# Kernel optimization log

Measured on AMD Instinct MI355X. Metric: run time of the kernel, lower is better.

## Reference

```python
import jax, jax.numpy as jnp
import numpy as np

M = 20          # mixture components
T = 1.0         # temperature
LATENT = 128
STROKE = 5
IN_DIM = LATENT + STROKE   # conditional=False -> 133
H = 1024        # dec_hidden_dim
HY = 256        # dec_hyper_dim
F = 64          # feature_dim (hypernet embedding)
NSEQ = 128      # Nmax
B = 64          # batch_size
OUT_DIM = 6 * M + 3
SQRT_T = float(np.sqrt(T))


def _w(key, shape, fan):
    return jax.random.normal(key, shape, jnp.float32) * np.float32(1.0 / np.sqrt(fan))


def setup_inputs() -> dict:
    key = jax.random.key(0)
    ks = jax.random.split(key, 16)
    inp = {
        'z': jax.random.normal(ks[0], (B, LATENT), jnp.float32),
        'strokes': jax.random.normal(ks[1], (NSEQ, B, IN_DIM), jnp.float32),
        'fc_in_w': _w(ks[2], (LATENT, 2 * H + 2 * HY), LATENT),
        'fc_in_b': jnp.zeros((2 * H + 2 * HY,), jnp.float32),
        'fc_proj_w': _w(ks[3], (H, OUT_DIM), H),
        'fc_proj_b': jnp.zeros((OUT_DIM,), jnp.float32),
        'Wx': _w(ks[4], (IN_DIM, 4 * H), IN_DIM),
        'Wh': _w(ks[5], (H, 4 * H), H),
        'b0': jnp.zeros((4, H), jnp.float32),
        'Wxh_hy': _w(ks[6], (IN_DIM + H, 4 * HY), IN_DIM + H),
        'Whh_hy': _w(ks[7], (HY, 4 * HY), HY),
        'b_hy': jnp.zeros((4 * HY,), jnp.float32),
        'Wzx': _w(ks[8], (HY, 4 * F), HY),
        'bzx': jnp.ones((4 * F,), jnp.float32),
        'Wzh': _w(ks[9], (HY, 4 * F), HY),
        'bzh': jnp.ones((4 * F,), jnp.float32),
        'Wzb': _w(ks[10], (HY, 4 * F), HY),
        'Dx': _w(ks[11], (4, F, H), F),
        'Dh': _w(ks[12], (4, F, H), F),
        'Db': _w(ks[13], (4, F, H), F),
    }
    return inp


def _hyperlstm_mdn(z, strokes, fc_in_w, fc_in_b, fc_proj_w, fc_proj_b, Wx, Wh, b0,
                   Wxh_hy, Whh_hy, b_hy, Wzx, bzx, Wzh, bzh, Wzb, Dx, Dh, Db):
    # initial states: tanh(fc_in(z)) split into [H, H, HY, HY]
    s0 = jnp.tanh(z @ fc_in_w + fc_in_b)
    h0, c0, hh0, ch0 = jnp.split(s0, [H, 2 * H, 2 * H + HY], axis=1)

    def step(carry, x_t):
        h, c, hh, ch = carry
        # hyper LSTM: plain LSTM over concat(x, h_main)
        hx = jnp.concatenate([x_t, h], axis=1)          # (B, IN_DIM+H)
        g = hx @ Wxh_hy + hh @ Whh_hy + b_hy            # (B, 4*HY)
        hi, hf, hg, ho = jnp.split(g, 4, axis=1)
        ch = jax.nn.sigmoid(hf) * ch + jax.nn.sigmoid(hi) * jnp.tanh(hg)
        hh = jax.nn.sigmoid(ho) * jnp.tanh(ch)
        # hyper embeddings -> per-gate row scales of main LSTM weights
        zx = (hh @ Wzx + bzx).reshape(-1, 4, F)
        zh = (hh @ Wzh + bzh).reshape(-1, 4, F)
        zb = (hh @ Wzb).reshape(-1, 4, F)
        sx = jnp.einsum('bgf,gfh->bgh', zx, Dx)         # (B,4,H)
        sh = jnp.einsum('bgf,gfh->bgh', zh, Dh)
        sb = jnp.einsum('bgf,gfh->bgh', zb, Db)
        pre = (sx * (x_t @ Wx).reshape(-1, 4, H)
               + sh * (h @ Wh).reshape(-1, 4, H)
               + sb + b0)                               # (B,4,H)
        mi, mf, mg, mo = pre[:, 0], pre[:, 1], pre[:, 2], pre[:, 3]
        c = jax.nn.sigmoid(mf) * c + jax.nn.sigmoid(mi) * jnp.tanh(mg)
        h = jax.nn.sigmoid(mo) * jnp.tanh(c)
        return (h, c, hh, ch), h

    _, outs = jax.lax.scan(step, (h0, c0, hh0, ch0), strokes)   # (NSEQ, B, H)

    dec = outs @ fc_proj_w + fc_proj_b                  # (NSEQ, B, 6M+3)
    # torch.split(dec,6,2) then stack(dim=1) -> (N, M, B, 6)
    mix = dec[..., :6 * M].reshape(NSEQ, B, M, 6).transpose(0, 2, 1, 3)
    # NOTE: source softmaxes mixture_weights over a size-1 axis -> all ones; reproduced faithfully
    mw = jax.nn.softmax(mix[..., 0:1] / T, axis=3)
    mean_x = mix[..., 1:2]
    mean_y = mix[..., 2:3]
    std_x = jnp.exp(mix[..., 3:4]) * SQRT_T
    std_y = jnp.exp(mix[..., 4:5]) * SQRT_T
    corr_xy = jnp.tanh(mix[..., 5:6])
    pen_state = jax.nn.softmax(dec[..., 6 * M:] / T, axis=2)    # (NSEQ, B, 3)
    return mw, mean_x, mean_y, std_x, std_y, corr_xy, pen_state


def reference(z, strokes, fc_in_w, fc_in_b, fc_proj_w, fc_proj_b, Wx, Wh, b0,
              Wxh_hy, Whh_hy, b_hy, Wzx, bzx, Wzh, bzh, Wzb, Dx, Dh, Db):
    return _hyperlstm_mdn(z, strokes, fc_in_w, fc_in_b, fc_proj_w, fc_proj_b, Wx, Wh, b0,
                          Wxh_hy, Whh_hy, b_hy, Wzx, bzx, Wzh, bzh, Wzb, Dx, Dh, Db)
```

## Files before the change

### kernel.cpp

```cpp
#include <hip/hip_runtime.h>

#define MM     20
#define LATENT 128
#define IN_DIM 133
#define HD     1024
#define HD4    4096
#define HY     256
#define FF     64
#define NSEQ   128
#define BB     64
#define OUT_DIM 123

typedef __attribute__((ext_vector_type(8))) short short8v;
typedef __attribute__((ext_vector_type(4))) float f32x4v;

__device__ float  g_c    [BB * HD];
__device__ float  g_ch   [BB * HY];
__device__ float  g_xT   [NSEQ * 192 * BB];
__device__ float  g_hWh  [8][BB * HD4];
__device__ float  g_gH   [8][BB * HD];
__device__ float  g_ghh  [2][BB * HD];
__device__ float  g_z    [BB * 3 * HY];
__device__ float  g_proj [8][BB * 128];
__device__ float  g_xWxA [NSEQ][BB * HD4];
__device__ float  g_gxA  [NSEQ][BB * HD];
__device__ unsigned short g_hRowHi [BB * HD],  g_hRowLo [BB * HD];
__device__ unsigned short g_hhRowHi[BB * HY],  g_hhRowLo[BB * HY];
__device__ unsigned short pkWhHi[32 * 256 * 512], pkWhLo[32 * 256 * 512];
__device__ unsigned short pkGhHi[32 *  64 * 512], pkGhLo[32 *  64 * 512];
__device__ unsigned short pkHhHi[ 8 *  64 * 512], pkHhLo[ 8 *  64 * 512];
__device__ unsigned short pkPjHi[32 *   8 * 512], pkPjLo[32 *   8 * 512];

__device__ __forceinline__ float sigf(float x) { return 1.0f / (1.0f + expf(-x)); }

__device__ __forceinline__ unsigned short bf16hi(float x) {
    union { float f; unsigned u; } v; v.f = x;
    unsigned r = v.u + 0x7FFFu + ((v.u >> 16) & 1u);
    return (unsigned short)(r >> 16);
}
__device__ __forceinline__ float bf16f(unsigned short h) {
    union { unsigned u; float f; } v; v.u = ((unsigned)h) << 16;
    return v.f;
}
__device__ __forceinline__ void bf16pair(float x, unsigned short* hi, unsigned short* lo) {
    unsigned short h = bf16hi(x);
    *hi = h;
    *lo = bf16hi(x - bf16f(h));
}

__device__ __forceinline__ void gload_lds16(const float* g, float* l) {
    __builtin_amdgcn_global_load_lds(
        (const __attribute__((address_space(1))) void*)g,
        (__attribute__((address_space(3))) void*)l, 16, 0, 0);
}

__global__ __launch_bounds__(256) void init_kernel(
    const float* __restrict__ z, const float* __restrict__ fc_in_w,
    const float* __restrict__ fc_in_b)
{
    int b = blockIdx.x, tid = threadIdx.x;
    __shared__ float zs[LATENT];
    if (tid < LATENT) zs[tid] = z[b * LATENT + tid];
    __syncthreads();
    for (int j = tid; j < 2560; j += 256) {
        float acc = fc_in_b[j];
        #pragma unroll 4
        for (int k = 0; k < LATENT; k++) acc += zs[k] * fc_in_w[k * 2560 + j];
        float s = tanhf(acc);
        if (j < 1024) {
            bf16pair(s, &g_hRowHi[b * HD + j], &g_hRowLo[b * HD + j]);
        } else if (j < 2048) {
            g_c[b * 1024 + (j - 1024)] = s;
        } else if (j < 2304) {
            int jj = j - 2048;
            bf16pair(s, &g_hhRowHi[b * HY + jj], &g_hhRowLo[b * HY + jj]);
        } else {
            g_ch[b * 256 + (j - 2304)] = s;
        }
    }
}

__global__ __launch_bounds__(256) void xt_kernel(const float* __restrict__ strokes)
{
    int t = blockIdx.x, tid = threadIdx.x;
    for (int i = tid; i < 192 * 64; i += 256) {
        int k = i >> 6, b = i & 63;
        g_xT[t * 192 * 64 + i] =
            (k < IN_DIM) ? strokes[(t * BB + b) * IN_DIM + k] : 0.f;
    }
}

__global__ __launch_bounds__(512) void pack_kernel(
    const float* __restrict__ Wh, const float* __restrict__ Wxh_hy,
    const float* __restrict__ Whh_hy, const float* __restrict__ fc_proj_w)
{
    int f = blockIdx.x, tid = threadIdx.x;
    int l = tid >> 3, j = tid & 7;
    int kk = ((l >> 4) << 3) + j, cc = l & 15;
    float val; unsigned short *hi, *lo;
    if (f < 8192) {
        int s = f >> 8, n = f & 255;
        val = Wh[(s * 32 + kk) * HD4 + n * 16 + cc];
        hi = &pkWhHi[f * 512 + tid]; lo = &pkWhLo[f * 512 + tid];
    } else if (f < 10240) {
        int f2 = f - 8192, s = f2 >> 6, n = f2 & 63;
        val = Wxh_hy[(133 + s * 32 + kk) * HD + n * 16 + cc];
        hi = &pkGhHi[f2 * 512 + tid]; lo = &pkGhLo[f2 * 512 + tid];
    } else if (f < 10752) {
        int f2 = f - 10240, s = f2 >> 6, n = f2 & 63;
        val = Whh_hy[(s * 32 + kk) * HD + n * 16 + cc];
        hi = &pkHhHi[f2 * 512 + tid]; lo = &pkHhLo[f2 * 512 + tid];
    } else {
        int f2 = f - 10752, s = f2 >> 3, n = f2 & 7;
        int c = n * 16 + cc;
        val = (c < OUT_DIM) ? fc_proj_w[(s * 32 + kk) * OUT_DIM + c] : 0.f;
        hi = &pkPjHi[f2 * 512 + tid]; lo = &pkPjLo[f2 * 512 + tid];
    }
    bf16pair(val, hi, lo);
}

template<int NTW>
__device__ __forceinline__ void mfma_gemm(
    const unsigned short* __restrict__ aHi, const unsigned short* __restrict__ aLo,
    int lda,
    const unsigned short* __restrict__ pHi, const unsigned short* __restrict__ pLo,
    int ntTot, int s0, int ns, int n0,
    float* __restrict__ Op, int ldo, int tid)
{
    int w = tid >> 6, l = tid & 63;
    int mt = w & 3, nh = w >> 2;
    int b0 = (mt << 4) + (l & 15);
    int kj = (l >> 4) << 3;
    f32x4v acc[NTW];
    #pragma unroll
    for (int i = 0; i < NTW; i++) acc[i] = (f32x4v){0.f, 0.f, 0.f, 0.f};
    for (int s = 0; s < ns; s++) {
        int sg = s0 + s;
        int koff = (sg << 5) + kj;
        short8v ah = *(const short8v*)(aHi + b0 * lda + koff);
        short8v al = *(const short8v*)(aLo + b0 * lda + koff);
        long fb = ((long)(sg * ntTot + n0 + nh * NTW) << 9) + (l << 3);
        #pragma unroll
        for (int nt = 0; nt < NTW; nt++) {
            short8v bh = *(const short8v*)(pHi + fb + (nt << 9));
            short8v bl = *(const short8v*)(pLo + fb + (nt << 9));
            acc[nt] = __builtin_amdgcn_mfma_f32_16x16x32_bf16(ah, bh, acc[nt], 0, 0, 0);
            acc[nt] = __builtin_amdgcn_mfma_f32_16x16x32_bf16(al, bh, acc[nt], 0, 0, 0);
            acc[nt] = __builtin_amdgcn_mfma_f32_16x16x32_bf16(ah, bl, acc[nt], 0, 0, 0);
        }
    }
    int rb = (mt << 4) + ((l >> 4) << 2);
    int cb = (n0 + nh * NTW) * 16 + (l & 15);
    #pragma unroll
    for (int nt = 0; nt < NTW; nt++) {
        #pragma unroll
        for (int j = 0; j < 4; j++)
            Op[(rb + j) * ldo + cb + (nt << 4)] = acc[nt][j];
    }
}

__global__ __launch_bounds__(512) void ka_kernel(int t)
{
    int u = blockIdx.x, tid = threadIdx.x;
    if (u < 128) {
        if (t < NSEQ) {
            int ch = u >> 4, ct = u & 15;
            mfma_gemm<8>(g_hRowHi, g_hRowLo, HD, pkWhHi, pkWhLo, 256,
                         ch * 4, 4, ct * 16, g_hWh[ch], HD4, tid);
        }
    } else if (u < 160) {
        if (t < NSEQ) {
            int i = u - 128, ch = i >> 2, ct = i & 3;
            mfma_gemm<8>(g_hRowHi, g_hRowLo, HD, pkGhHi, pkGhLo, 64,
                         ch * 4, 4, ct * 16, g_gH[ch], HD, tid);
        }
    } else if (u < 168) {
        if (t < NSEQ) {
            int i = u - 160, ch = i >> 2, ct = i & 3;
            mfma_gemm<8>(g_hhRowHi, g_hhRowLo, HY, pkHhHi, pkHhLo, 64,
                         ch * 4, 4, ct * 16, g_ghh[ch], HD, tid);
        }
    } else {
        if (t > 0) {
            int ch = u - 168;
            mfma_gemm<4>(g_hRowHi, g_hRowLo, HD, pkPjHi, pkPjLo, 8,
                         ch * 4, 4, 0, g_proj[ch], 128, tid);
        }
    }
}

__device__ __forceinline__ void stage128(const float* Wp, int ldw, int wrows,
                                         int co, int pn, float* dst, int tid)
{
    #pragma unroll
    for (int q = 0; q < 2; q++) {
        int s = (q << 9) + tid;
        int r = s >> 5, c4 = s & 31;
        int kr = (pn << 5) + r; if (kr >= wrows) kr = wrows - 1;
        gload_lds16(Wp + kr * ldw + co + (c4 << 2), dst + (s << 2));
    }
}
__device__ __forceinline__ void gemm128(
    const float* AT, const float* Wp, int ldw, int wrows, int co, int np,
    float* Op, int ldo, float* pool, int tid)
{
    int cq = tid & 31, bq = tid >> 5;
    float4 acc0 = {0,0,0,0}, acc1 = {0,0,0,0}, acc2 = {0,0,0,0}, acc3 = {0,0,0,0};
    stage128(Wp, ldw, wrows, co, 0, pool, tid);
    for (int pn = 0; pn < np; pn++) {
        __syncthreads();
        if (pn + 1 < np)
            stage128(Wp, ldw, wrows, co, pn + 1, pool + (((pn + 1) & 1) << 12), tid);
        const float* Ap2 = AT + (pn << 11) + (bq << 2);
        const float* Wcc = pool + ((pn & 1) << 12) + (cq << 2);
        #pragma unroll 8
        for (int k = 0; k < 32; k++) {
            float4 a = *(const float4*)(Ap2 + (k << 6));
            float4 w = *(const float4*)(Wcc + (k << 7));
            acc0.x += a.x*w.x; acc0.y += a.x*w.y; acc0.z += a.x*w.z; acc0.w += a.x*w.w;
            acc1.x += a.y*w.x; acc1.y += a.y*w.y; acc1.z += a.y*w.z; acc1.w += a.y*w.w;
            acc2.x += a.z*w.x; acc2.y += a.z*w.y; acc2.z += a.z*w.z; acc2.w += a.z*w.w;
            acc3.x += a.w*w.x; acc3.y += a.w*w.y; acc3.z += a.w*w.z; acc3.w += a.w*w.w;
        }
    }
    float* op = Op + (bq << 2) * ldo + co + (cq << 2);
    *(float4*)(op)           = acc0;  *(float4*)(op + ldo)     = acc1;
    *(float4*)(op + 2 * ldo) = acc2;  *(float4*)(op + 3 * ldo) = acc3;
}

__global__ __launch_bounds__(512, 2) void pre_kernel(
    const float* __restrict__ Wx, const float* __restrict__ Wxh_hy)
{
    __shared__ float pool[8192];
    int u = blockIdx.x, tid = threadIdx.x;
    if (u < 4096) {
        int t = u >> 5, ct = u & 31;
        gemm128(g_xT + t * 192 * 64, Wx, HD4, IN_DIM, ct * 128, 5,
                g_xWxA[t], HD4, pool, tid);
    } else {
        int i = u - 4096, t = i >> 3, ct = i & 7;
        gemm128(g_xT + t * 192 * 64, Wxh_hy, HD, IN_DIM, ct * 128, 5,
                g_gxA[t], HD, pool, tid);
    }
}

__global__ __launch_bounds__(1024) void k2_kernel(
    const float* __restrict__ b_hy,
    const float* __restrict__ Wzx, const float* __restrict__ bzx,
    const float* __restrict__ Wzh, const float* __restrict__ bzh,
    const float* __restrict__ Wzb,
    const float* __restrict__ fc_proj_b, float* __restrict__ out, int t)
{
    __shared__ float gsum[1024];
    __shared__ float hhB[256];
    int blk = blockIdx.x, tid = threadIdx.x;
    if (blk < 64) {
        if (t >= NSEQ) return;
        int b = blk, base = b * HD;
        {
            int j = tid;
            float a = b_hy[j] + g_gxA[t][base + j];
            #pragma unroll
            for (int c = 0; c < 8; c++) a += g_gH[c][base + j];
            a += g_ghh[0][base + j] + g_ghh[1][base + j];
            gsum[j] = a;
        }
        __syncthreads();
        if (tid < 256) {
            float gi = gsum[tid],       gf = gsum[256 + tid];
            float gg = gsum[512 + tid], go = gsum[768 + tid];
            float ch = g_ch[b * HY + tid];
            ch = sigf(gf) * ch + sigf(gi) * tanhf(gg);
            float hh = sigf(go) * tanhf(ch);
            g_ch[b * HY + tid] = ch;
            bf16pair(hh, &g_hhRowHi[b * HY + tid], &g_hhRowLo[b * HY + tid]);
            hhB[tid] = hh;
        }
        __syncthreads();
        if (tid < 768) {
            int ten = tid >> 8, oo = tid & 255;
            const float* Wz = (ten == 0) ? Wzx : (ten == 1) ? Wzh : Wzb;
            float acc = (ten == 0) ? bzx[oo] : (ten == 1) ? bzh[oo] : 0.f;
            #pragma unroll 8
            for (int k = 0; k < HY; k++) acc += hhB[k] * Wz[(k << 8) + oo];
            g_z[b * 768 + tid] = acc;
        }
    } else {
        if (t == 0) return;
        int b = blk - 64, tp = t - 1, base7 = b << 7;
        int c = tid;
        if (c < 120) {
            float v = fc_proj_b[c];
            #pragma unroll
            for (int q = 0; q < 8; q++) v += g_proj[q][base7 + c];
            int m = c / 6, r = c - m * 6;
            int oidx = tp * (MM * BB) + m * BB + b;
            if      (r == 0) out[oidx]          = 1.0f;
            else if (r == 1) out[163840 + oidx] = v;
            else if (r == 2) out[327680 + oidx] = v;
            else if (r == 3) out[491520 + oidx] = expf(v);
            else if (r == 4) out[655360 + oidx] = expf(v);
            else             out[819200 + oidx] = tanhf(v);
        } else if (c == 120) {
            float p0 = fc_proj_b[120], p1 = fc_proj_b[121], p2 = fc_proj_b[122];
            #pragma unroll
            for (int q = 0; q < 8; q++) {
                p0 += g_proj[q][base7 + 120];
                p1 += g_proj[q][base7 + 121];
                p2 += g_proj[q][base7 + 122];
            }
            float mx = fmaxf(p0, fmaxf(p1, p2));
            float e0 = expf(p0 - mx), e1 = expf(p1 - mx), e2 = expf(p2 - mx);
            float s = e0 + e1 + e2;
            int ob = 983040 + tp * (BB * 3) + b * 3;
            out[ob + 0] = e0 / s; out[ob + 1] = e1 / s; out[ob + 2] = e2 / s;
        }
    }
}

__global__ __launch_bounds__(512) void k3_kernel(
    const float* __restrict__ Dx, const float* __restrict__ Dh,
    const float* __restrict__ Db, const float* __restrict__ b0w, int t)
{
    __shared__ float zC[6144];
    __shared__ float preC[1024];
    int blk = blockIdx.x, tid = threadIdx.x;
    int bg = blk >> 5, sl = blk & 31;
    int hi0 = sl << 5;
    {
        const float4* src = (const float4*)(g_z + bg * 8 * 768);
        float4* dst = (float4*)zC;
        for (int i = tid; i < 1536; i += 512) dst[i] = src[i];
    }
    __syncthreads();
    int hi_l = tid & 31, gq = (tid >> 5) & 3, b4 = tid >> 7;
    int hi = hi0 + hi_l;
    const float* dxp = Dx + gq * 64 * HD + hi;
    const float* dhp = Dh + gq * 64 * HD + hi;
    const float* dbp = Db + gq * 64 * HD + hi;
    const float* z0 = zC + b4 * 768;
    const float* z1 = zC + (b4 + 4) * 768;
    int zo = gq << 6;
    float ax0 = 0.f, ah0 = 0.f, ab0 = 0.f, ax1 = 0.f, ah1 = 0.f, ab1 = 0.f;
    #pragma unroll 4
    for (int f = 0; f < FF; f++) {
        float dx = dxp[f * HD], dh = dhp[f * HD], db = dbp[f * HD];
        ax0 += z0[zo + f] * dx; ah0 += z0[256 + zo + f] * dh;
        ab0 += z0[512 + zo + f] * db;
        ax1 += z1[zo + f] * dx; ah1 += z1[256 + zo + f] * dh;
        ab1 += z1[512 + zo + f] * db;
    }
    int idx = (gq << 10) + hi;
    int b0i = (bg << 3) + b4, b1i = b0i + 4;
    float hw0 = 0.f, hw1 = 0.f;
    #pragma unroll
    for (int q = 0; q < 8; q++) {
        hw0 += g_hWh[q][b0i * HD4 + idx];
        hw1 += g_hWh[q][b1i * HD4 + idx];
    }
    float xw0 = g_xWxA[t][b0i * HD4 + idx], xw1 = g_xWxA[t][b1i * HD4 + idx];
    float bw = b0w[idx];
    float pre0 = ax0 * xw0 + ah0 * hw0 + ab0 + bw;
    float pre1 = ax1 * xw1 + ah1 * hw1 + ab1 + bw;
    preC[((b4 << 2) + gq) * 32 + hi_l]       = pre0;
    preC[(((b4 + 4) << 2) + gq) * 32 + hi_l] = pre1;
    __syncthreads();
    if (tid < 256) {
        int bi = tid >> 5, hl = tid & 31;
        int b8 = (bg << 3) + bi, ha = b8 * HD + hi0 + hl;
        float pi = preC[((bi << 2) + 0) * 32 + hl];
        float pf = preC[((bi << 2) + 1) * 32 + hl];
        float pg = preC[((bi << 2) + 2) * 32 + hl];
        float po = preC[((bi << 2) + 3) * 32 + hl];
        float cv = g_c[ha];
        float nc = sigf(pf) * cv + sigf(pi) * tanhf(pg);
        float nh = sigf(po) * tanhf(nc);
        g_c[ha] = nc;
        bf16pair(nh, &g_hRowHi[ha], &g_hRowLo[ha]);
    }
}

extern "C" void kernel_launch(void* const* d_in, const int* in_sizes, int n_in,
                              void* d_out, int out_size, void* d_ws, size_t ws_size,
                              hipStream_t stream)
{
    const float* z         = (const float*)d_in[0];
    const float* strokes   = (const float*)d_in[1];
    const float* fc_in_w   = (const float*)d_in[2];
    const float* fc_in_b   = (const float*)d_in[3];
    const float* fc_proj_w = (const float*)d_in[4];
    const float* fc_proj_b = (const float*)d_in[5];
    const float* Wx        = (const float*)d_in[6];
    const float* Wh        = (const float*)d_in[7];
    const float* b0w       = (const float*)d_in[8];
    const float* Wxh_hy    = (const float*)d_in[9];
    const float* Whh_hy    = (const float*)d_in[10];
    const float* b_hy      = (const float*)d_in[11];
    const float* Wzx       = (const float*)d_in[12];
    const float* bzx       = (const float*)d_in[13];
    const float* Wzh       = (const float*)d_in[14];
    const float* bzh       = (const float*)d_in[15];
    const float* Wzb       = (const float*)d_in[16];
    const float* Dx        = (const float*)d_in[17];
    const float* Dh        = (const float*)d_in[18];
    const float* Db        = (const float*)d_in[19];
    (void)d_ws; (void)ws_size; (void)in_sizes; (void)n_in; (void)out_size;
    float* out = (float*)d_out;

    init_kernel<<<64, 256, 0, stream>>>(z, fc_in_w, fc_in_b);
    xt_kernel<<<128, 256, 0, stream>>>(strokes);
    pack_kernel<<<11008, 512, 0, stream>>>(Wh, Wxh_hy, Whh_hy, fc_proj_w);
    pre_kernel<<<5120, 512, 0, stream>>>(Wx, Wxh_hy);
    for (int t = 0; t < NSEQ; t++) {
        ka_kernel<<<176, 512, 0, stream>>>(t);
        k2_kernel<<<128, 1024, 0, stream>>>(b_hy, Wzx, bzx, Wzh, bzh, Wzb,
                                            fc_proj_b, out, t);
        k3_kernel<<<256, 512, 0, stream>>>(Dx, Dh, Db, b0w, t);
    }
    ka_kernel<<<176, 512, 0, stream>>>(NSEQ);
    k2_kernel<<<128, 1024, 0, stream>>>(b_hy, Wzx, bzx, Wzh, bzh, Wzb,
                                        fc_proj_b, out, NSEQ);
}
```

Baseline: 5.990 ms.

## Fuse hyper-LSTM update and hypernet modulation kernels with per-batch flag sync

Merges k2 and k3 into one kernel launched per timestep. 64 blocks compute the hyper-LSTM cell and z embeddings, then publish a per-batch release flag. 256 further blocks spread the output projection across threads, then spin on those flags before computing the D-projection modulation. This removes one kernel launch and one grid-wide barrier per step. In exchange it relies on all 320 blocks being co-resident to avoid deadlock, and it narrows the k2 blocks to 512 threads.

```diff
diff --git a/kernel.cpp b/kernel.cpp
--- a/kernel.cpp
+++ b/kernel.cpp
@@ -24,6 +24,7 @@
 __device__ float  g_proj [8][BB * 128];
 __device__ float  g_xWxA [NSEQ][BB * HD4];
 __device__ float  g_gxA  [NSEQ][BB * HD];
+__device__ int    g_flag [BB];
 __device__ unsigned short g_hRowHi [BB * HD],  g_hRowLo [BB * HD];
 __device__ unsigned short g_hhRowHi[BB * HY],  g_hhRowLo[BB * HY];
 __device__ unsigned short pkWhHi[32 * 256 * 512], pkWhLo[32 * 256 * 512];
@@ -59,6 +60,7 @@
     const float* __restrict__ fc_in_b)
 {
     int b = blockIdx.x, tid = threadIdx.x;
+    if (b == 0 && tid < BB) g_flag[tid] = 0;
     __shared__ float zs[LATENT];
     if (tid < LATENT) zs[tid] = z[b * LATENT + tid];
     __syncthreads();
@@ -244,21 +246,26 @@
     }
 }
 
-__global__ __launch_bounds__(1024) void k2_kernel(
+__global__ __launch_bounds__(512) void kb_kernel(
     const float* __restrict__ b_hy,
     const float* __restrict__ Wzx, const float* __restrict__ bzx,
     const float* __restrict__ Wzh, const float* __restrict__ bzh,
     const float* __restrict__ Wzb,
+    const float* __restrict__ Dx, const float* __restrict__ Dh,
+    const float* __restrict__ Db, const float* __restrict__ b0w,
     const float* __restrict__ fc_proj_b, float* __restrict__ out, int t)
 {
-    __shared__ float gsum[1024];
-    __shared__ float hhB[256];
+    __shared__ float pool[7168];
     int blk = blockIdx.x, tid = threadIdx.x;
+
     if (blk < 64) {
         if (t >= NSEQ) return;
+        float* gsum = pool;
+        float* hhB  = pool + 1024;
         int b = blk, base = b * HD;
-        {
-            int j = tid;
+        #pragma unroll
+        for (int half = 0; half < 2; half++) {
+            int j = (half << 9) + tid;
             float a = b_hy[j] + g_gxA[t][base + j];
             #pragma unroll
             for (int c = 0; c < 8; c++) a += g_gH[c][base + j];
@@ -277,18 +284,28 @@
             hhB[tid] = hh;
         }
         __syncthreads();
-        if (tid < 768) {
-            int ten = tid >> 8, oo = tid & 255;
+        for (int o = tid; o < 768; o += 512) {
+            int ten = o >> 8, oo = o & 255;
             const float* Wz = (ten == 0) ? Wzx : (ten == 1) ? Wzh : Wzb;
             float acc = (ten == 0) ? bzx[oo] : (ten == 1) ? bzh[oo] : 0.f;
             #pragma unroll 8
             for (int k = 0; k < HY; k++) acc += hhB[k] * Wz[(k << 8) + oo];
-            g_z[b * 768 + tid] = acc;
-        }
-    } else {
-        if (t == 0) return;
-        int b = blk - 64, tp = t - 1, base7 = b << 7;
-        int c = tid;
+            g_z[b * 768 + o] = acc;
+        }
+        __syncthreads();
+        if (tid == 0) {
+            __threadfence();
+            __hip_atomic_store(&g_flag[b], t + 1, __ATOMIC_RELEASE,
+                               __HIP_MEMORY_SCOPE_AGENT);
+        }
+        return;
+    }
+
+    int i = blk - 64, bg = i >> 5, sl = i & 31;
+    if (t > 0 && tid < 31) {
+        int it = i * 31 + tid;
+        int b = it / 124, c = it - b * 124;
+        int tp = t - 1, base7 = b << 7;
         if (c < 120) {
             float v = fc_proj_b[c];
             #pragma unroll
@@ -316,23 +333,24 @@
             out[ob + 0] = e0 / s; out[ob + 1] = e1 / s; out[ob + 2] = e2 / s;
         }
     }
-}
-
-__global__ __launch_bounds__(512) void k3_kernel(
-    const float* __restrict__ Dx, const float* __restrict__ Dh,
-    const float* __restrict__ Db, const float* __restrict__ b0w, int t)
-{
-    __shared__ float zC[6144];
-    __shared__ float preC[1024];
-    int blk = blockIdx.x, tid = threadIdx.x;
-    int bg = blk >> 5, sl = blk & 31;
-    int hi0 = sl << 5;
+    if (t >= NSEQ) return;
+
+    if (tid < 8) {
+        while (__hip_atomic_load(&g_flag[(bg << 3) + tid], __ATOMIC_ACQUIRE,
+                                 __HIP_MEMORY_SCOPE_AGENT) < t + 1)
+            __builtin_amdgcn_s_sleep(4);
+    }
+    __syncthreads();
+
+    float* zC   = pool;
+    float* preC = pool + 6144;
     {
         const float4* src = (const float4*)(g_z + bg * 8 * 768);
         float4* dst = (float4*)zC;
-        for (int i = tid; i < 1536; i += 512) dst[i] = src[i];
+        for (int q = tid; q < 1536; q += 512) dst[q] = src[q];
     }
     __syncthreads();
+    int hi0 = sl << 5;
     int hi_l = tid & 31, gq = (tid >> 5) & 3, b4 = tid >> 7;
     int hi = hi0 + hi_l;
     const float* dxp = Dx + gq * 64 * HD + hi;
@@ -413,11 +431,10 @@
     pre_kernel<<<5120, 512, 0, stream>>>(Wx, Wxh_hy);
     for (int t = 0; t < NSEQ; t++) {
         ka_kernel<<<176, 512, 0, stream>>>(t);
-        k2_kernel<<<128, 1024, 0, stream>>>(b_hy, Wzx, bzx, Wzh, bzh, Wzb,
-                                            fc_proj_b, out, t);
-        k3_kernel<<<256, 512, 0, stream>>>(Dx, Dh, Db, b0w, t);
+        kb_kernel<<<320, 512, 0, stream>>>(b_hy, Wzx, bzx, Wzh, bzh, Wzb,
+                                           Dx, Dh, Db, b0w, fc_proj_b, out, t);
     }
     ka_kernel<<<176, 512, 0, stream>>>(NSEQ);
-    k2_kernel<<<128, 1024, 0, stream>>>(b_hy, Wzx, bzx, Wzh, bzh, Wzb,
-                                        fc_proj_b, out, NSEQ);
-}
+    kb_kernel<<<320, 512, 0, stream>>>(b_hy, Wzx, bzx, Wzh, bzh, Wzb,
+                                       Dx, Dh, Db, b0w, fc_proj_b, out, NSEQ);
+}
```

After: 20.81 ms. 247% more time.

## Fuse hyper-LSTM and main LSTM update kernels into one per-step kernel

Applied to the files above, without the earlier changes.

Merges the hyper-LSTM/z-projection kernel and the main LSTM gate kernel into a single kernel where each block handles two batch rows and half the hidden units, keeping z in shared memory. Hyper-LSTM state is double-buffered so duplicate computation across the two halves is race-free. This removes one launch per timestep and the global z round trip, at the cost of a smaller grid, redundant hyper work, and more total reads of the D matrices.

```diff
diff --git a/kernel.cpp b/kernel.cpp
--- a/kernel.cpp
+++ b/kernel.cpp
@@ -15,12 +15,11 @@
 typedef __attribute__((ext_vector_type(4))) float f32x4v;
 
 __device__ float  g_c    [BB * HD];
-__device__ float  g_ch   [BB * HY];
+__device__ float  g_chP  [2][BB * HY];
 __device__ float  g_xT   [NSEQ * 192 * BB];
 __device__ float  g_hWh  [8][BB * HD4];
 __device__ float  g_gH   [8][BB * HD];
 __device__ float  g_ghh  [2][BB * HD];
-__device__ float  g_z    [BB * 3 * HY];
 __device__ float  g_proj [8][BB * 128];
 __device__ float  g_xWxA [NSEQ][BB * HD4];
 __device__ float  g_gxA  [NSEQ][BB * HD];
@@ -75,7 +74,7 @@
             int jj = j - 2048;
             bf16pair(s, &g_hhRowHi[b * HY + jj], &g_hhRowLo[b * HY + jj]);
         } else {
-            g_ch[b * 256 + (j - 2304)] = s;
+            g_chP[0][b * 256 + (j - 2304)] = s;
         }
     }
 }
@@ -244,51 +243,25 @@
     }
 }
 
-__global__ __launch_bounds__(1024) void k2_kernel(
+__global__ __launch_bounds__(1024) void kb_kernel(
     const float* __restrict__ b_hy,
     const float* __restrict__ Wzx, const float* __restrict__ bzx,
     const float* __restrict__ Wzh, const float* __restrict__ bzh,
     const float* __restrict__ Wzb,
+    const float* __restrict__ Dx, const float* __restrict__ Dh,
+    const float* __restrict__ Db, const float* __restrict__ b0w,
     const float* __restrict__ fc_proj_b, float* __restrict__ out, int t)
 {
-    __shared__ float gsum[1024];
-    __shared__ float hhB[256];
+    __shared__ float gsum[2][1024];
+    __shared__ float hhL [2][256];
+    __shared__ float zC  [2][768];
+    __shared__ float preC[2][4][512];
     int blk = blockIdx.x, tid = threadIdx.x;
-    if (blk < 64) {
-        if (t >= NSEQ) return;
-        int b = blk, base = b * HD;
-        {
-            int j = tid;
-            float a = b_hy[j] + g_gxA[t][base + j];
-            #pragma unroll
-            for (int c = 0; c < 8; c++) a += g_gH[c][base + j];
-            a += g_ghh[0][base + j] + g_ghh[1][base + j];
-            gsum[j] = a;
-        }
-        __syncthreads();
-        if (tid < 256) {
-            float gi = gsum[tid],       gf = gsum[256 + tid];
-            float gg = gsum[512 + tid], go = gsum[768 + tid];
-            float ch = g_ch[b * HY + tid];
-            ch = sigf(gf) * ch + sigf(gi) * tanhf(gg);
-            float hh = sigf(go) * tanhf(ch);
-            g_ch[b * HY + tid] = ch;
-            bf16pair(hh, &g_hhRowHi[b * HY + tid], &g_hhRowLo[b * HY + tid]);
-            hhB[tid] = hh;
-        }
-        __syncthreads();
-        if (tid < 768) {
-            int ten = tid >> 8, oo = tid & 255;
-            const float* Wz = (ten == 0) ? Wzx : (ten == 1) ? Wzh : Wzb;
-            float acc = (ten == 0) ? bzx[oo] : (ten == 1) ? bzh[oo] : 0.f;
-            #pragma unroll 8
-            for (int k = 0; k < HY; k++) acc += hhB[k] * Wz[(k << 8) + oo];
-            g_z[b * 768 + tid] = acc;
-        }
-    } else {
-        if (t == 0) return;
-        int b = blk - 64, tp = t - 1, base7 = b << 7;
-        int c = tid;
+    int bp = blk >> 1, half = blk & 1;
+    int bA = bp << 1;
+
+    if (t > 0 && tid < 124) {
+        int b = blk, c = tid, tp = t - 1, base7 = b << 7;
         if (c < 120) {
             float v = fc_proj_b[c];
             #pragma unroll
@@ -316,62 +289,86 @@
             out[ob + 0] = e0 / s; out[ob + 1] = e1 / s; out[ob + 2] = e2 / s;
         }
     }
-}
-
-__global__ __launch_bounds__(512) void k3_kernel(
-    const float* __restrict__ Dx, const float* __restrict__ Dh,
-    const float* __restrict__ Db, const float* __restrict__ b0w, int t)
-{
-    __shared__ float zC[6144];
-    __shared__ float preC[1024];
-    int blk = blockIdx.x, tid = threadIdx.x;
-    int bg = blk >> 5, sl = blk & 31;
-    int hi0 = sl << 5;
+    if (t >= NSEQ) return;
+    int par = t & 1;
+
+    #pragma unroll
+    for (int b2 = 0; b2 < 2; b2++) {
+        int base = (bA + b2) * HD, j = tid;
+        float a = b_hy[j] + g_gxA[t][base + j];
+        #pragma unroll
+        for (int c = 0; c < 8; c++) a += g_gH[c][base + j];
+        a += g_ghh[0][base + j] + g_ghh[1][base + j];
+        gsum[b2][j] = a;
+    }
+    __syncthreads();
+    if (tid < 512) {
+        int b2 = tid >> 8, e = tid & 255, b = bA + b2;
+        float gi = gsum[b2][e],       gf = gsum[b2][256 + e];
+        float gg = gsum[b2][512 + e], go = gsum[b2][768 + e];
+        float ch = g_chP[par][b * HY + e];
+        ch = sigf(gf) * ch + sigf(gi) * tanhf(gg);
+        float hh = sigf(go) * tanhf(ch);
+        hhL[b2][e] = hh;
+        if (half == 0) {
+            g_chP[par ^ 1][b * HY + e] = ch;
+            bf16pair(hh, &g_hhRowHi[b * HY + e], &g_hhRowLo[b * HY + e]);
+        }
+    }
+    __syncthreads();
+    for (int o = tid; o < 1536; o += 1024) {
+        int b2 = (o >= 768) ? 1 : 0;
+        int oz = o - (b2 ? 768 : 0);
+        int ten = oz >> 8, col = oz & 255;
+        const float* Wz = (ten == 0) ? Wzx : (ten == 1) ? Wzh : Wzb;
+        float acc = (ten == 0) ? bzx[col] : (ten == 1) ? bzh[col] : 0.f;
+        #pragma unroll 8
+        for (int k = 0; k < HY; k++) acc += hhL[b2][k] * Wz[(k << 8) + col];
+        zC[b2][oz] = acc;
+    }
+    __syncthreads();
     {
-        const float4* src = (const float4*)(g_z + bg * 8 * 768);
-        float4* dst = (float4*)zC;
-        for (int i = tid; i < 1536; i += 512) dst[i] = src[i];
+        int b2 = tid >> 9, gq = (tid >> 7) & 3, h4 = tid & 127;
+        int hi = (half << 9) + (h4 << 2);
+        const float* zrow = &zC[b2][gq << 6];
+        const float* dxp = Dx + (gq << 6) * HD + hi;
+        const float* dhp = Dh + (gq << 6) * HD + hi;
+        const float* dbp = Db + (gq << 6) * HD + hi;
+        float4 ax = {0,0,0,0}, ah = {0,0,0,0}, ab = {0,0,0,0};
+        #pragma unroll 4
+        for (int f = 0; f < FF; f++) {
+            float zx = zrow[f], zh = zrow[256 + f], zb = zrow[512 + f];
+            float4 dx = *(const float4*)(dxp + f * HD);
+            float4 dh = *(const float4*)(dhp + f * HD);
+            float4 db = *(const float4*)(dbp + f * HD);
+            ax.x += zx * dx.x; ax.y += zx * dx.y; ax.z += zx * dx.z; ax.w += zx * dx.w;
+            ah.x += zh * dh.x; ah.y += zh * dh.y; ah.z += zh * dh.z; ah.w += zh * dh.w;
+            ab.x += zb * db.x; ab.y += zb * db.y; ab.z += zb * db.z; ab.w += zb * db.w;
+        }
+        int idx = (gq << 10) + hi;
+        int b = bA + b2;
+        float4 hw = {0,0,0,0};
+        #pragma unroll
+        for (int q = 0; q < 8; q++) {
+            float4 p = *(const float4*)(&g_hWh[q][b * HD4 + idx]);
+            hw.x += p.x; hw.y += p.y; hw.z += p.z; hw.w += p.w;
+        }
+        float4 xw = *(const float4*)(&g_xWxA[t][b * HD4 + idx]);
+        float4 bw = *(const float4*)(&b0w[idx]);
+        float4 pre;
+        pre.x = ax.x * xw.x + ah.x * hw.x + ab.x + bw.x;
+        pre.y = ax.y * xw.y + ah.y * hw.y + ab.y + bw.y;
+        pre.z = ax.z * xw.z + ah.z * hw.z + ab.z + bw.z;
+        pre.w = ax.w * xw.w + ah.w * hw.w + ab.w + bw.w;
+        *(float4*)(&preC[b2][gq][h4 << 2]) = pre;
     }
     __syncthreads();
-    int hi_l = tid & 31, gq = (tid >> 5) & 3, b4 = tid >> 7;
-    int hi = hi0 + hi_l;
-    const float* dxp = Dx + gq * 64 * HD + hi;
-    const float* dhp = Dh + gq * 64 * HD + hi;
-    const float* dbp = Db + gq * 64 * HD + hi;
-    const float* z0 = zC + b4 * 768;
-    const float* z1 = zC + (b4 + 4) * 768;
-    int zo = gq << 6;
-    float ax0 = 0.f, ah0 = 0.f, ab0 = 0.f, ax1 = 0.f, ah1 = 0.f, ab1 = 0.f;
-    #pragma unroll 4
-    for (int f = 0; f < FF; f++) {
-        float dx = dxp[f * HD], dh = dhp[f * HD], db = dbp[f * HD];
-        ax0 += z0[zo + f] * dx; ah0 += z0[256 + zo + f] * dh;
-        ab0 += z0[512 + zo + f] * db;
-        ax1 += z1[zo + f] * dx; ah1 += z1[256 + zo + f] * dh;
-        ab1 += z1[512 + zo + f] * db;
-    }
-    int idx = (gq << 10) + hi;
-    int b0i = (bg << 3) + b4, b1i = b0i + 4;
-    float hw0 = 0.f, hw1 = 0.f;
-    #pragma unroll
-    for (int q = 0; q < 8; q++) {
-        hw0 += g_hWh[q][b0i * HD4 + idx];
-        hw1 += g_hWh[q][b1i * HD4 + idx];
-    }
-    float xw0 = g_xWxA[t][b0i * HD4 + idx], xw1 = g_xWxA[t][b1i * HD4 + idx];
-    float bw = b0w[idx];
-    float pre0 = ax0 * xw0 + ah0 * hw0 + ab0 + bw;
-    float pre1 = ax1 * xw1 + ah1 * hw1 + ab1 + bw;
-    preC[((b4 << 2) + gq) * 32 + hi_l]       = pre0;
-    preC[(((b4 + 4) << 2) + gq) * 32 + hi_l] = pre1;
-    __syncthreads();
-    if (tid < 256) {
-        int bi = tid >> 5, hl = tid & 31;
-        int b8 = (bg << 3) + bi, ha = b8 * HD + hi0 + hl;
-        float pi = preC[((bi << 2) + 0) * 32 + hl];
-        float pf = preC[((bi << 2) + 1) * 32 + hl];
-        float pg = preC[((bi << 2) + 2) * 32 + hl];
-        float po = preC[((bi << 2) + 3) * 32 + hl];
+    {
+        int b2 = tid >> 9, hl = tid & 511;
+        int b = bA + b2;
+        int ha = b * HD + (half << 9) + hl;
+        float pi = preC[b2][0][hl], pf = preC[b2][1][hl];
+        float pg = preC[b2][2][hl], po = preC[b2][3][hl];
         float cv = g_c[ha];
         float nc = sigf(pf) * cv + sigf(pi) * tanhf(pg);
         float nh = sigf(po) * tanhf(nc);
@@ -413,11 +410,10 @@
     pre_kernel<<<5120, 512, 0, stream>>>(Wx, Wxh_hy);
     for (int t = 0; t < NSEQ; t++) {
         ka_kernel<<<176, 512, 0, stream>>>(t);
-        k2_kernel<<<128, 1024, 0, stream>>>(b_hy, Wzx, bzx, Wzh, bzh, Wzb,
-                                            fc_proj_b, out, t);
-        k3_kernel<<<256, 512, 0, stream>>>(Dx, Dh, Db, b0w, t);
+        kb_kernel<<<64, 1024, 0, stream>>>(b_hy, Wzx, bzx, Wzh, bzh, Wzb,
+                                           Dx, Dh, Db, b0w, fc_proj_b, out, t);
     }
     ka_kernel<<<176, 512, 0, stream>>>(NSEQ);
-    k2_kernel<<<128, 1024, 0, stream>>>(b_hy, Wzx, bzx, Wzh, bzh, Wzb,
-                                        fc_proj_b, out, NSEQ);
-}
+    kb_kernel<<<64, 1024, 0, stream>>>(b_hy, Wzx, bzx, Wzh, bzh, Wzb,
+                                       Dx, Dh, Db, b0w, fc_proj_b, out, NSEQ);
+}
```

Result: slower. 8.832 ms (+47.4%).
